# Kernel optimization log

Measured on AMD Instinct MI355X. Metric: run time of the kernel, lower is better.

Reference implementation:

```python
import jax, jax.numpy as jnp
import numpy as np

B, S, DIM = 2, 2048, 2048
H, DN, DR, DV, L = 16, 128, 64, 128, 512  # heads, nope, rope, v, kv_lora_rank
EPS = 1e-5


def setup_inputs() -> dict:
    key = jax.random.key(0)
    ks = jax.random.split(key, 12)
    x = jax.random.normal(ks[0], (B, S, DIM), dtype=jnp.float32)
    # rotary tables (DeepSeek-style: theta = 10000^{-2i/d})
    inv_freq = 1.0 / (10000.0 ** (jnp.arange(0, DR, 2, dtype=jnp.float32) / DR))
    ang = jnp.arange(S, dtype=jnp.float32)[:, None] * inv_freq[None, :]  # [S, DR/2]
    freqs_cos = jnp.cos(ang)
    freqs_sin = jnp.sin(ang)
    w = 0.02
    wq_w = jax.random.normal(ks[1], (H * (DN + DR), DIM), dtype=jnp.float32) * w
    wq_b = jnp.zeros((H * (DN + DR),), dtype=jnp.float32)
    wkv_a_w = jax.random.normal(ks[2], (L + DR, DIM), dtype=jnp.float32) * w
    wkv_a_b = jnp.zeros((L + DR,), dtype=jnp.float32)
    kv_norm_g = jnp.ones((L,), dtype=jnp.float32)
    kv_norm_b = jnp.zeros((L,), dtype=jnp.float32)
    wkv_b_w = jax.random.normal(ks[3], (H * (DN + DV), L), dtype=jnp.float32) * w
    wo_w = jax.random.normal(ks[4], (DIM, H * DV), dtype=jnp.float32) * w
    wo_b = jnp.zeros((DIM,), dtype=jnp.float32)
    return {"x": x, "start_pos": 0, "freqs_cos": freqs_cos, "freqs_sin": freqs_sin,
            "wq_w": wq_w, "wq_b": wq_b, "wkv_a_w": wkv_a_w, "wkv_a_b": wkv_a_b,
            "kv_norm_g": kv_norm_g, "kv_norm_b": kv_norm_b, "wkv_b_w": wkv_b_w,
            "wo_w": wo_w, "wo_b": wo_b}


def _rope(t, cos, sin):
    # t: [B, S, n, DR] interpreted as interleaved (re, im) pairs
    tr = t.reshape(*t.shape[:-1], DR // 2, 2)
    re, im = tr[..., 0], tr[..., 1]
    c = cos[None, :, None, :]
    s = sin[None, :, None, :]
    out = jnp.stack([re * c - im * s, re * s + im * c], axis=-1)
    return out.reshape(t.shape)


def _layernorm(v, g, b):
    mu = jnp.mean(v, axis=-1, keepdims=True)
    var = jnp.mean(jnp.square(v - mu), axis=-1, keepdims=True)
    return (v - mu) * jax.lax.rsqrt(var + EPS) * g + b


def reference(x, start_pos, freqs_cos, freqs_sin, wq_w, wq_b, wkv_a_w, wkv_a_b,
              kv_norm_g, kv_norm_b, wkv_b_w, wo_w, wo_b):
    bsz, seqlen, _ = x.shape
    scale = (DN + DR) ** -0.5
    # q projection
    q = (x @ wq_w.T + wq_b).reshape(bsz, seqlen, H, DN + DR)
    q_nope, q_pe = q[..., :DN], q[..., DN:]
    q_pe = _rope(q_pe, freqs_cos, freqs_sin)
    # kv projection
    kv_full = x @ wkv_a_w.T + wkv_a_b
    kv, k_pe = kv_full[..., :L], kv_full[..., L:]
    k_pe = _rope(k_pe[:, :, None, :], freqs_cos, freqs_sin)[:, :, 0, :]  # [B,S,DR]
    kvn = _layernorm(kv, kv_norm_g, kv_norm_b)  # compressed kv cache entries [B,S,L]
    wkv_b = wkv_b_w.reshape(H, DN + DV, L)
    # absorption: fold wkv_b's k-part into q_nope
    q_abs = jnp.einsum('bshd,hdc->bshc', q_nope, wkv_b[:, :DN])
    scores = (jnp.einsum('bshc,btc->bsht', q_abs, kvn)
              + jnp.einsum('bshr,btr->bsht', q_pe, k_pe)) * scale
    # causal mask (query global pos = start_pos + s, key pos = t)
    qpos = jnp.arange(seqlen) + start_pos
    tpos = jnp.arange(seqlen)
    causal = qpos[:, None] >= tpos[None, :]  # [S, T]
    scores = jnp.where(causal[None, :, None, :], scores, -jnp.inf)
    p = jax.nn.softmax(scores.astype(jnp.float32), axis=-1).astype(x.dtype)
    # compressed attention output then un-absorb v
    ctx = jnp.einsum('bsht,btc->bshc', p, kvn)
    out = jnp.einsum('bshc,hdc->bshd', ctx, wkv_b[:, -DV:])
    return out.reshape(bsz, seqlen, H * DV) @ wo_w.T + wo_b
```

## Files before the change

kernel.cpp:

```cpp
#include <hip/hip_runtime.h>
#include <stdint.h>

typedef __attribute__((ext_vector_type(8))) __bf16 bf16x8;
typedef __attribute__((ext_vector_type(4))) float  f32x4;
typedef __attribute__((ext_vector_type(8))) unsigned short u16x8;
typedef __attribute__((ext_vector_type(2))) unsigned int u32x2;
typedef __attribute__((ext_vector_type(4))) unsigned int u32x4;

typedef __attribute__((address_space(1))) void AS1void;
typedef __attribute__((address_space(3))) void AS3void;
typedef __attribute__((address_space(3))) const unsigned char AS3c;

__device__ __forceinline__ float b2f(unsigned short u) {
  unsigned x = ((unsigned)u) << 16; float f; __builtin_memcpy(&f, &x, 4); return f;
}
__device__ __forceinline__ unsigned short f2b(float f) {
  unsigned x; __builtin_memcpy(&x, &f, 4);
  unsigned r = (x + 0x7fffu + ((x >> 16) & 1u)) >> 16;
  return (unsigned short)r;
}
__device__ __forceinline__ void gload16(const void* g, void* l) {
  __builtin_amdgcn_global_load_lds((AS1void*)(void*)g, (AS3void*)l, 16, 0, 0);
}
__device__ __forceinline__ bf16x8 mk8(u32x2 a, u32x2 b) {
  u32x4 t; t[0] = a[0]; t[1] = a[1]; t[2] = b[0]; t[3] = b[1];
  bf16x8 r; __builtin_memcpy(&r, &t, 16); return r;
}
template<int OFF>
__device__ __forceinline__ u32x2 tr_read(AS3c* vp) {
  u32x2 r;
  asm volatile("ds_read_b64_tr_b16 %0, %1 offset:%2"
               : "=&v"(r) : "v"(vp), "n"(OFF));
  return r;
}

__global__ __launch_bounds__(256) void k_cast(const float* __restrict__ in,
                                              unsigned short* __restrict__ out, long n) {
  long i = ((long)blockIdx.x * 256 + threadIdx.x) * 4;
  if (i >= n) return;
  float4 v = *(const float4*)(in + i);
  ushort4 o;
  o.x = f2b(v.x); o.y = f2b(v.y); o.z = f2b(v.z); o.w = f2b(v.w);
  *(ushort4*)(out + i) = o;
}

__global__ __launch_bounds__(256) void k_prep_wkvb(const float* __restrict__ wkvb,
                                                   unsigned short* __restrict__ kT,
                                                   unsigned short* __restrict__ vv) {
  long i = (long)blockIdx.x * 256 + threadIdx.x;
  {
    int d = (int)(i & 127); long r = i >> 7; int c = (int)(r & 511); int h = (int)(r >> 9);
    kT[i] = f2b(wkvb[((long)(h * 256 + d)) * 512 + c]);
  }
  {
    int c = (int)(i & 511); long r = i >> 9; int d = (int)(r & 127); int h = (int)(r >> 7);
    vv[i] = f2b(wkvb[((long)(h * 256 + 128 + d)) * 512 + c]);
  }
}

template<int OUTF32, int BIAS>
__global__ __launch_bounds__(256, 4) void k_gemm_bt(
    const unsigned short* __restrict__ A, long lda, long aSb, long aSh,
    const unsigned short* __restrict__ B, long ldb, long bSb, long bSh,
    void* __restrict__ Cp, long ldc, long cSb, long cSh,
    const float* __restrict__ bias,
    int M, int N, int K, int zH) {
  __shared__ __align__(16) unsigned short sA[128 * 32];
  __shared__ __align__(16) unsigned short sB[128 * 32];
  const int z = blockIdx.z, zb = z / zH, zh = z % zH;
  const unsigned short* Ab = A + zb * aSb + zh * aSh;
  const unsigned short* Bb = B + zb * bSb + zh * bSh;
  const long cOff = (long)zb * cSb + (long)zh * cSh;
  const int n0 = blockIdx.x * 128, m0 = blockIdx.y * 128;
  const int t = threadIdx.x, w = t >> 6, l = t & 63;
  const int wr = (w >> 1) * 64, wc = (w & 1) * 64;
  const int lr = l & 15, lg = l >> 4;
  f32x4 acc[4][4] = {};
  for (int k0 = 0; k0 < K; k0 += 32) {
    #pragma unroll
    for (int cc = 0; cc < 2; ++cc) {
      int c = t + cc * 256;
      int row = c >> 2, col = (c & 3) * 8;
      int ar = m0 + row; ar = ar < M ? ar : M - 1;
      int br = n0 + row; br = br < N ? br : N - 1;
      gload16(Ab + (long)ar * lda + k0 + col, (char*)sA + c * 16);
      gload16(Bb + (long)br * ldb + k0 + col, (char*)sB + c * 16);
    }
    __syncthreads();
    bf16x8 af[4], bf[4];
    #pragma unroll
    for (int i = 0; i < 4; ++i) af[i] = *(const bf16x8*)&sA[(wr + i * 16 + lr) * 32 + lg * 8];
    #pragma unroll
    for (int j = 0; j < 4; ++j) bf[j] = *(const bf16x8*)&sB[(wc + j * 16 + lr) * 32 + lg * 8];
    #pragma unroll
    for (int i = 0; i < 4; ++i)
      #pragma unroll
      for (int j = 0; j < 4; ++j)
        acc[i][j] = __builtin_amdgcn_mfma_f32_16x16x32_bf16(af[i], bf[j], acc[i][j], 0, 0, 0);
    __syncthreads();
  }
  #pragma unroll
  for (int i = 0; i < 4; ++i) {
    #pragma unroll
    for (int r = 0; r < 4; ++r) {
      int row = m0 + wr + i * 16 + lg * 4 + r;
      if (row >= M) continue;
      #pragma unroll
      for (int j = 0; j < 4; ++j) {
        int col = n0 + wc + j * 16 + lr;
        if (col >= N) continue;
        float v = acc[i][j][r];
        if (BIAS) v += bias[col];
        if (OUTF32) ((float*)Cp)[cOff + (long)row * ldc + col] = v;
        else ((unsigned short*)Cp)[cOff + (long)row * ldc + col] = f2b(v);
      }
    }
  }
}

__global__ __launch_bounds__(256) void k_ln(const unsigned short* __restrict__ kvb,
                                            const float* __restrict__ g,
                                            const float* __restrict__ be,
                                            unsigned short* __restrict__ kcat) {
  const int w = threadIdx.x >> 6, l = threadIdx.x & 63;
  const long row = (long)blockIdx.x * 4 + w;
  const unsigned short* src = kvb + row * 576 + l * 8;
  u16x8 v = *(const u16x8*)src;
  float f[8]; float s = 0.f, s2 = 0.f;
  #pragma unroll
  for (int j = 0; j < 8; ++j) { f[j] = b2f(v[j]); s += f[j]; s2 += f[j] * f[j]; }
  #pragma unroll
  for (int m = 1; m < 64; m <<= 1) { s += __shfl_xor(s, m); s2 += __shfl_xor(s2, m); }
  float mu = s * (1.f / 512.f);
  float var = s2 * (1.f / 512.f) - mu * mu;
  float rs = rsqrtf(var + 1e-5f);
  u16x8 o;
  #pragma unroll
  for (int j = 0; j < 8; ++j) {
    int c = l * 8 + j;
    o[j] = f2b((f[j] - mu) * rs * g[c] + be[c]);
  }
  *(u16x8*)(kcat + row * 576 + l * 8) = o;
}

__global__ __launch_bounds__(256) void k_rope_k(const unsigned short* __restrict__ kvb,
                                                const float* __restrict__ fc,
                                                const float* __restrict__ fs,
                                                unsigned short* __restrict__ kcat) {
  int i = blockIdx.x * 256 + threadIdx.x;
  int p = i & 31; int r = i >> 5;
  int s = r & 2047; int b = r >> 11;
  long base = ((long)(b * 2048 + s)) * 576 + 512 + 2 * p;
  float re = b2f(kvb[base]), im = b2f(kvb[base + 1]);
  float c = fc[s * 32 + p], sn = fs[s * 32 + p];
  kcat[base] = f2b(re * c - im * sn);
  kcat[base + 1] = f2b(re * sn + im * c);
}

__global__ __launch_bounds__(256) void k_rope_q(const unsigned short* __restrict__ qfull,
                                                const float* __restrict__ fc,
                                                const float* __restrict__ fs,
                                                unsigned short* __restrict__ qcat) {
  long i = (long)blockIdx.x * 256 + threadIdx.x;
  int p = (int)(i & 31); long r = i >> 5;
  int h = (int)(r & 15); r >>= 4;
  int s = (int)(r & 2047); int b = (int)(r >> 11);
  const unsigned short* src = qfull + ((long)(b * 2048 + s)) * 3072 + h * 192 + 128 + 2 * p;
  float re = b2f(src[0]), im = b2f(src[1]);
  float c = fc[s * 32 + p], sn = fs[s * 32 + p];
  unsigned short* dst = qcat + ((long)((b * 16 + h) * 2048 + s)) * 576 + 512 + 2 * p;
  dst[0] = f2b(re * c - im * sn);
  dst[1] = f2b(re * sn + im * c);
}

__global__ __launch_bounds__(256, 2) void k_attn(
    const unsigned short* __restrict__ qcat,
    const unsigned short* __restrict__ kcat,
    unsigned short* __restrict__ ctx,
    const int* __restrict__ spp) {
  __shared__ __align__(16) char smem[41248];
  const int id = blockIdx.x;
  const int rr = id & 7;
  const int b = rr >> 2;
  const int local = (id >> 3) * 4 + (rr & 3);
  const int qb = 31 - (local >> 4);
  const int h = local & 15;
  const int t = threadIdx.x, w = t >> 6, l = t & 63;
  const int lq = l & 15, hh = l >> 4;
  const int sp = spp[0];
  const long bh = (long)(b * 16 + h);
  const long qrow0 = bh * 2048 + qb * 64 + w * 16;
  const float scale = 0.07216878364870323f;

  bf16x8 qf[18];
  #pragma unroll
  for (int kk = 0; kk < 18; ++kk)
    qf[kk] = *(const bf16x8*)&qcat[(qrow0 + lq) * 576 + kk * 32 + hh * 8];

  f32x4 acc[8][4];
  #pragma unroll
  for (int i = 0; i < 8; ++i)
    #pragma unroll
    for (int j = 0; j < 4; ++j) acc[i][j] = (f32x4){0.f, 0.f, 0.f, 0.f};
  float mrun = -1e30f, lrun = 0.f;
  const int qg = qb * 64 + w * 16 + lq + sp;
  int tmax = qb * 64 + 63 + sp; if (tmax > 2047) tmax = 2047;

  const unsigned short* kbase = kcat + (long)b * 2048 * 576;

  unsigned short* sP = (unsigned short*)(smem + 36864);
  float* sAl = (float*)(smem + 40960);
  int* sNeed = (int*)(smem + 41216);
  const int qrow = w * 16 + lq;
  const int xq = ((qrow >> 1) & 3) << 4;
  const int vcol = (hh * 16) ^ (((lq >> 1) & 3) << 4);
  const int kq = ((lq >> 2) << 7) + ((lq & 3) << 5) + ((hh & 1) << 4) + ((hh >> 1) << 10);

  for (int t0 = 0; t0 <= tmax; t0 += 32) {
    #pragma unroll
    for (int cc = 0; cc < 9; ++cc) {
      int c = t + cc * 256;
      int tt = ((c >> 3) & 7) * 4 + ((c >> 1) & 3);
      int gc = (c >> 6) * 16 + (c & 1) * 8;
      gload16(kbase + (long)(t0 + tt) * 576 + gc, smem + c * 16);
    }
    asm volatile("s_waitcnt vmcnt(0)" ::: "memory");
    __builtin_amdgcn_sched_barrier(0);
    __builtin_amdgcn_s_barrier();
    __builtin_amdgcn_sched_barrier(0);

    f32x4 sc[2];
    sc[0] = (f32x4){0.f,0.f,0.f,0.f}; sc[1] = (f32x4){0.f,0.f,0.f,0.f};
    __builtin_amdgcn_s_setprio(1);
    #pragma unroll
    for (int tf = 0; tf < 2; ++tf) {
      const char* rb = smem + kq + tf * 512;
      #pragma unroll
      for (int kk = 0; kk < 18; ++kk) {
        bf16x8 kf = *(const bf16x8*)(rb + kk * 2048);
        sc[tf] = __builtin_amdgcn_mfma_f32_16x16x32_bf16(kf, qf[kk], sc[tf], 0, 0, 0);
      }
    }
    __builtin_amdgcn_s_setprio(0);

    float v[2][4];
    float mt = -1e30f;
    #pragma unroll
    for (int tf = 0; tf < 2; ++tf)
      #pragma unroll
      for (int r = 0; r < 4; ++r) {
        int tg = t0 + tf * 16 + 4 * hh + r;
        v[tf][r] = (tg <= qg) ? sc[tf][r] * scale : -1e30f;
        mt = fmaxf(mt, v[tf][r]);
      }
    mt = fmaxf(mt, __shfl_xor(mt, 16));
    mt = fmaxf(mt, __shfl_xor(mt, 32));
    float al = 1.f;
    unsigned long long needb = __ballot(mt > mrun + 8.f);
    if (needb) {
      float mn = fmaxf(mrun, mt);
      al = __expf(mrun - mn);
      mrun = mn;
      lrun *= al;
    }
    float sr = 0.f;
    #pragma unroll
    for (int tf = 0; tf < 2; ++tf) {
      ushort4 pk;
      float e0 = __expf(v[tf][0] - mrun);
      float e1 = __expf(v[tf][1] - mrun);
      float e2 = __expf(v[tf][2] - mrun);
      float e3 = __expf(v[tf][3] - mrun);
      sr += (e0 + e1) + (e2 + e3);
      pk.x = f2b(e0); pk.y = f2b(e1); pk.z = f2b(e2); pk.w = f2b(e3);
      *(ushort4*)((char*)sP + qrow * 64 + ((32 * tf + 8 * hh) ^ xq)) = pk;
    }
    sr += __shfl_xor(sr, 16);
    sr += __shfl_xor(sr, 32);
    lrun += sr;
    if (l < 16) sAl[w * 16 + l] = al;
    if (l == 0) sNeed[w] = needb ? 1 : 0;
    asm volatile("s_waitcnt lgkmcnt(0)" ::: "memory");
    __builtin_amdgcn_sched_barrier(0);
    __builtin_amdgcn_s_barrier();
    __builtin_amdgcn_sched_barrier(0);

    int needAny = sNeed[0] | sNeed[1] | sNeed[2] | sNeed[3];
    if (needAny) {
      float a4[4];
      #pragma unroll
      for (int q2 = 0; q2 < 4; ++q2) a4[q2] = sAl[q2 * 16 + lq];
      #pragma unroll
      for (int cb = 0; cb < 8; ++cb)
        #pragma unroll
        for (int q2 = 0; q2 < 4; ++q2) acc[cb][q2] *= a4[q2];
    }
    bf16x8 pf0 = *(const bf16x8*)((char*)sP + (0 * 16 + lq) * 64 + vcol);
    bf16x8 pf1 = *(const bf16x8*)((char*)sP + (1 * 16 + lq) * 64 + vcol);
    bf16x8 pf2 = *(const bf16x8*)((char*)sP + (2 * 16 + lq) * 64 + vcol);
    bf16x8 pf3 = *(const bf16x8*)((char*)sP + (3 * 16 + lq) * 64 + vcol);
    __builtin_amdgcn_sched_barrier(0);
    AS3c* vp3 = (AS3c*)(smem + (w * 8192) + hh * 256 + lq * 8);
    u32x2 A0, A1, B0, B1, C0, C1, D0, D1;
    #define TRR2(d0, d1, CB) do { \
      d0 = tr_read<(CB) * 1024>(vp3); \
      d1 = tr_read<(CB) * 1024 + 128>(vp3); } while (0)
    #define PVC(CB, E0, E1) do { \
      bf16x8 vf = mk8(E0, E1); \
      acc[CB][0] = __builtin_amdgcn_mfma_f32_16x16x32_bf16(vf, pf0, acc[CB][0], 0, 0, 0); \
      acc[CB][1] = __builtin_amdgcn_mfma_f32_16x16x32_bf16(vf, pf1, acc[CB][1], 0, 0, 0); \
      acc[CB][2] = __builtin_amdgcn_mfma_f32_16x16x32_bf16(vf, pf2, acc[CB][2], 0, 0, 0); \
      acc[CB][3] = __builtin_amdgcn_mfma_f32_16x16x32_bf16(vf, pf3, acc[CB][3], 0, 0, 0); } while (0)
    TRR2(A0, A1, 0); TRR2(B0, B1, 1);
    TRR2(C0, C1, 2); TRR2(D0, D1, 3);
    asm volatile("s_waitcnt lgkmcnt(4)" ::: "memory");
    __builtin_amdgcn_sched_barrier(0);
    __builtin_amdgcn_s_setprio(1);
    PVC(0, A0, A1); PVC(1, B0, B1);
    __builtin_amdgcn_s_setprio(0);
    TRR2(A0, A1, 4); TRR2(B0, B1, 5);
    asm volatile("s_waitcnt lgkmcnt(4)" ::: "memory");
    __builtin_amdgcn_sched_barrier(0);
    __builtin_amdgcn_s_setprio(1);
    PVC(2, C0, C1); PVC(3, D0, D1);
    __builtin_amdgcn_s_setprio(0);
    TRR2(C0, C1, 6); TRR2(D0, D1, 7);
    asm volatile("s_waitcnt lgkmcnt(4)" ::: "memory");
    __builtin_amdgcn_sched_barrier(0);
    __builtin_amdgcn_s_setprio(1);
    PVC(4, A0, A1); PVC(5, B0, B1);
    __builtin_amdgcn_s_setprio(0);
    asm volatile("s_waitcnt lgkmcnt(0)" ::: "memory");
    __builtin_amdgcn_sched_barrier(0);
    __builtin_amdgcn_s_setprio(1);
    PVC(6, C0, C1); PVC(7, D0, D1);
    __builtin_amdgcn_s_setprio(0);
    #undef TRR2
    #undef PVC
    __builtin_amdgcn_sched_barrier(0);
    __builtin_amdgcn_s_barrier();
    __builtin_amdgcn_sched_barrier(0);
  }

  if (l < 16) sAl[w * 16 + l] = lrun;
  __syncthreads();
  float linv[4];
  #pragma unroll
  for (int q2 = 0; q2 < 4; ++q2) linv[q2] = 1.0f / sAl[q2 * 16 + lq];
  unsigned short* eb = (unsigned short*)smem;
  unsigned short* Co = ctx + (bh * 2048 + qb * 64) * 512;
  #pragma unroll
  for (int p = 0; p < 2; ++p) {
    __syncthreads();
    #pragma unroll
    for (int cb = 0; cb < 8; ++cb) {
      const int c0 = w * 128 + cb * 16 + hh * 4;
      #pragma unroll
      for (int q2 = 0; q2 < 2; ++q2) {
        int qq = p * 2 + q2;
        f32x4 a = acc[cb][qq];
        ushort4 o;
        o.x = f2b(a[0] * linv[qq]); o.y = f2b(a[1] * linv[qq]);
        o.z = f2b(a[2] * linv[qq]); o.w = f2b(a[3] * linv[qq]);
        *(ushort4*)&eb[(q2 * 16 + lq) * 528 + c0] = o;
      }
    }
    __syncthreads();
    #pragma unroll
    for (int i = 0; i < 8; ++i) {
      int id2 = t + i * 256;
      int row = id2 >> 6, col = (id2 & 63) * 8;
      *(u16x8*)&Co[(long)(p * 32 + row) * 512 + col] = *(const u16x8*)&eb[row * 528 + col];
    }
  }
}

extern "C" void kernel_launch(void* const* d_in, const int* in_sizes, int n_in,
                              void* d_out, int out_size, void* d_ws, size_t ws_size,
                              hipStream_t stream) {
  const float* x      = (const float*)d_in[0];
  const int*   sp     = (const int*)d_in[1];
  const float* fcos   = (const float*)d_in[2];
  const float* fsin   = (const float*)d_in[3];
  const float* wq_w   = (const float*)d_in[4];
  const float* wq_b   = (const float*)d_in[5];
  const float* wkva_w = (const float*)d_in[6];
  const float* wkva_b = (const float*)d_in[7];
  const float* lng    = (const float*)d_in[8];
  const float* lnb    = (const float*)d_in[9];
  const float* wkvb_w = (const float*)d_in[10];
  const float* wo_w   = (const float*)d_in[11];
  const float* wo_b   = (const float*)d_in[12];
  float* out = (float*)d_out;

  if (ws_size < 171180032) return;

  char* ws = (char*)d_ws;
  unsigned short* xb     = (unsigned short*)(ws + 0);
  unsigned short* wqbf   = (unsigned short*)(ws + 16777216);
  unsigned short* qfull  = (unsigned short*)(ws + 29360128);
  unsigned short* ctx    = (unsigned short*)(ws + 0);
  unsigned short* wkvabf = (unsigned short*)(ws + 67108864);
  unsigned short* wkvbkT = (unsigned short*)(ws + 69468160);
  unsigned short* wkvbv  = (unsigned short*)(ws + 71565312);
  unsigned short* wobf   = (unsigned short*)(ws + 73662464);
  unsigned short* kvbf   = (unsigned short*)(ws + 82051072);
  unsigned short* kcat   = (unsigned short*)(ws + 86769664);
  unsigned short* qcat   = (unsigned short*)(ws + 95682560);
  unsigned short* outh   = qcat;

  k_cast<<<8192, 256, 0, stream>>>(x, xb, 8388608L);
  k_cast<<<6144, 256, 0, stream>>>(wq_w, wqbf, 6291456L);
  k_cast<<<1152, 256, 0, stream>>>(wkva_w, wkvabf, 1179648L);
  k_cast<<<4096, 256, 0, stream>>>(wo_w, wobf, 4194304L);
  k_prep_wkvb<<<4096, 256, 0, stream>>>(wkvb_w, wkvbkT, wkvbv);

  k_gemm_bt<0, 1><<<dim3(24, 32, 1), 256, 0, stream>>>(
      xb, 2048, 0, 0, wqbf, 2048, 0, 0, qfull, 3072, 0, 0, wq_b, 4096, 3072, 2048, 1);
  k_gemm_bt<0, 1><<<dim3(5, 32, 1), 256, 0, stream>>>(
      xb, 2048, 0, 0, wkvabf, 2048, 0, 0, kvbf, 576, 0, 0, wkva_b, 4096, 576, 2048, 1);

  k_ln<<<1024, 256, 0, stream>>>(kvbf, lng, lnb, kcat);
  k_rope_k<<<512, 256, 0, stream>>>(kvbf, fcos, fsin, kcat);
  k_rope_q<<<16384, 256, 0, stream>>>(qfull, fcos, fsin, qcat);

  k_gemm_bt<0, 0><<<dim3(4, 16, 32), 256, 0, stream>>>(
      qfull, 3072, (long)2048 * 3072, 192,
      wkvbkT, 128, 0, (long)512 * 128,
      qcat, 576, (long)16 * 2048 * 576, (long)2048 * 576,
      nullptr, 2048, 512, 128, 16);

  k_attn<<<dim3(1024, 1, 1), 256, 0, stream>>>(qcat, kcat, ctx, sp);

  k_gemm_bt<0, 0><<<dim3(1, 16, 32), 256, 0, stream>>>(
      ctx, 512, (long)16 * 2048 * 512, (long)2048 * 512,
      wkvbv, 512, 0, (long)128 * 512,
      outh, 2048, (long)2048 * 2048, 128,
      nullptr, 2048, 128, 512, 16);

  k_gemm_bt<1, 1><<<dim3(16, 32, 1), 256, 0, stream>>>(
      outh, 2048, 0, 0, wobf, 2048, 0, 0, out, 2048, 0, 0, wo_b, 4096, 2048, 2048, 1);
}
```

Baseline: 635.3 us.

## Double attention key tile to 64 tokens per iteration in MLA kernel

Each attention loop iteration now stages 64 key/value rows (instead of 32) into LDS, halving the number of loop iterations, global-load waits and block barriers per KV pass. The QK loop is reordered to iterate over the contraction dimension outermost, the P tile widens to 128 bytes per row with a new XOR swizzle, and PV runs as two 32-token halves. An extra barrier is inserted after QK, and the epilogue writes all 64 output rows in one pass. LDS grows to about 74 KB, which may reduce blocks per CU versus the 2-wave launch bound, and causal blocks now process more masked tokens on the diagonal.

```diff
diff --git a/kernel.cpp b/kernel.cpp
--- a/kernel.cpp
+++ b/kernel.cpp
@@ -178,7 +178,7 @@
     const unsigned short* __restrict__ kcat,
     unsigned short* __restrict__ ctx,
     const int* __restrict__ spp) {
-  __shared__ __align__(16) char smem[41248];
+  __shared__ __align__(16) char smem[74112];
   const int id = blockIdx.x;
   const int rr = id & 7;
   const int b = rr >> 2;
@@ -208,45 +208,49 @@
 
   const unsigned short* kbase = kcat + (long)b * 2048 * 576;
 
-  unsigned short* sP = (unsigned short*)(smem + 36864);
-  float* sAl = (float*)(smem + 40960);
-  int* sNeed = (int*)(smem + 41216);
+  unsigned short* sP = (unsigned short*)(smem + 65536);
+  float* sAl = (float*)(smem + 73728);
+  int* sNeed = (int*)(smem + 73984);
   const int qrow = w * 16 + lq;
-  const int xq = ((qrow >> 1) & 3) << 4;
-  const int vcol = (hh * 16) ^ (((lq >> 1) & 3) << 4);
-  const int kq = ((lq >> 2) << 7) + ((lq & 3) << 5) + ((hh & 1) << 4) + ((hh >> 1) << 10);
-
-  for (int t0 = 0; t0 <= tmax; t0 += 32) {
-    #pragma unroll
-    for (int cc = 0; cc < 9; ++cc) {
-      int c = t + cc * 256;
-      int tt = ((c >> 3) & 7) * 4 + ((c >> 1) & 3);
-      int gc = (c >> 6) * 16 + (c & 1) * 8;
-      gload16(kbase + (long)(t0 + tt) * 576 + gc, smem + c * 16);
+  const int xq = (qrow & 7) << 4;
+  const int kq = ((hh >> 1) << 11) + ((lq >> 2) << 7) + ((lq & 3) << 5) + ((hh & 1) << 4);
+
+  for (int t0 = 0; t0 <= tmax; t0 += 64) {
+    #pragma unroll
+    for (int cc = 0; cc < 18; ++cc) {
+      int c2 = t + cc * 256;
+      int tt = ((c2 >> 3) & 15) * 4 + ((c2 >> 1) & 3);
+      int gc = (c2 >> 7) * 16 + (c2 & 1) * 8;
+      gload16(kbase + (long)(t0 + tt) * 576 + gc, smem + c2 * 16);
     }
     asm volatile("s_waitcnt vmcnt(0)" ::: "memory");
     __builtin_amdgcn_sched_barrier(0);
     __builtin_amdgcn_s_barrier();
     __builtin_amdgcn_sched_barrier(0);
 
-    f32x4 sc[2];
-    sc[0] = (f32x4){0.f,0.f,0.f,0.f}; sc[1] = (f32x4){0.f,0.f,0.f,0.f};
+    f32x4 sc[4];
+    #pragma unroll
+    for (int tf = 0; tf < 4; ++tf) sc[tf] = (f32x4){0.f, 0.f, 0.f, 0.f};
     __builtin_amdgcn_s_setprio(1);
     #pragma unroll
-    for (int tf = 0; tf < 2; ++tf) {
-      const char* rb = smem + kq + tf * 512;
-      #pragma unroll
-      for (int kk = 0; kk < 18; ++kk) {
-        bf16x8 kf = *(const bf16x8*)(rb + kk * 2048);
+    for (int kk = 0; kk < 18; ++kk) {
+      const char* rb = smem + kq + kk * 4096;
+      #pragma unroll
+      for (int tf = 0; tf < 4; ++tf) {
+        bf16x8 kf = *(const bf16x8*)(rb + tf * 512);
         sc[tf] = __builtin_amdgcn_mfma_f32_16x16x32_bf16(kf, qf[kk], sc[tf], 0, 0, 0);
       }
     }
     __builtin_amdgcn_s_setprio(0);
-
-    float v[2][4];
+    asm volatile("s_waitcnt lgkmcnt(0)" ::: "memory");
+    __builtin_amdgcn_sched_barrier(0);
+    __builtin_amdgcn_s_barrier();
+    __builtin_amdgcn_sched_barrier(0);
+
+    float v[4][4];
     float mt = -1e30f;
     #pragma unroll
-    for (int tf = 0; tf < 2; ++tf)
+    for (int tf = 0; tf < 4; ++tf)
       #pragma unroll
       for (int r = 0; r < 4; ++r) {
         int tg = t0 + tf * 16 + 4 * hh + r;
@@ -265,7 +269,7 @@
     }
     float sr = 0.f;
     #pragma unroll
-    for (int tf = 0; tf < 2; ++tf) {
+    for (int tf = 0; tf < 4; ++tf) {
       ushort4 pk;
       float e0 = __expf(v[tf][0] - mrun);
       float e1 = __expf(v[tf][1] - mrun);
@@ -273,7 +277,7 @@
       float e3 = __expf(v[tf][3] - mrun);
       sr += (e0 + e1) + (e2 + e3);
       pk.x = f2b(e0); pk.y = f2b(e1); pk.z = f2b(e2); pk.w = f2b(e3);
-      *(ushort4*)((char*)sP + qrow * 64 + ((32 * tf + 8 * hh) ^ xq)) = pk;
+      *(ushort4*)((char*)sP + qrow * 128 + ((32 * tf + 8 * hh) ^ xq)) = pk;
     }
     sr += __shfl_xor(sr, 16);
     sr += __shfl_xor(sr, 32);
@@ -295,48 +299,51 @@
         #pragma unroll
         for (int q2 = 0; q2 < 4; ++q2) acc[cb][q2] *= a4[q2];
     }
-    bf16x8 pf0 = *(const bf16x8*)((char*)sP + (0 * 16 + lq) * 64 + vcol);
-    bf16x8 pf1 = *(const bf16x8*)((char*)sP + (1 * 16 + lq) * 64 + vcol);
-    bf16x8 pf2 = *(const bf16x8*)((char*)sP + (2 * 16 + lq) * 64 + vcol);
-    bf16x8 pf3 = *(const bf16x8*)((char*)sP + (3 * 16 + lq) * 64 + vcol);
-    __builtin_amdgcn_sched_barrier(0);
-    AS3c* vp3 = (AS3c*)(smem + (w * 8192) + hh * 256 + lq * 8);
-    u32x2 A0, A1, B0, B1, C0, C1, D0, D1;
-    #define TRR2(d0, d1, CB) do { \
-      d0 = tr_read<(CB) * 1024>(vp3); \
-      d1 = tr_read<(CB) * 1024 + 128>(vp3); } while (0)
-    #define PVC(CB, E0, E1) do { \
-      bf16x8 vf = mk8(E0, E1); \
-      acc[CB][0] = __builtin_amdgcn_mfma_f32_16x16x32_bf16(vf, pf0, acc[CB][0], 0, 0, 0); \
-      acc[CB][1] = __builtin_amdgcn_mfma_f32_16x16x32_bf16(vf, pf1, acc[CB][1], 0, 0, 0); \
-      acc[CB][2] = __builtin_amdgcn_mfma_f32_16x16x32_bf16(vf, pf2, acc[CB][2], 0, 0, 0); \
-      acc[CB][3] = __builtin_amdgcn_mfma_f32_16x16x32_bf16(vf, pf3, acc[CB][3], 0, 0, 0); } while (0)
-    TRR2(A0, A1, 0); TRR2(B0, B1, 1);
-    TRR2(C0, C1, 2); TRR2(D0, D1, 3);
-    asm volatile("s_waitcnt lgkmcnt(4)" ::: "memory");
-    __builtin_amdgcn_sched_barrier(0);
-    __builtin_amdgcn_s_setprio(1);
-    PVC(0, A0, A1); PVC(1, B0, B1);
-    __builtin_amdgcn_s_setprio(0);
-    TRR2(A0, A1, 4); TRR2(B0, B1, 5);
-    asm volatile("s_waitcnt lgkmcnt(4)" ::: "memory");
-    __builtin_amdgcn_sched_barrier(0);
-    __builtin_amdgcn_s_setprio(1);
-    PVC(2, C0, C1); PVC(3, D0, D1);
-    __builtin_amdgcn_s_setprio(0);
-    TRR2(C0, C1, 6); TRR2(D0, D1, 7);
-    asm volatile("s_waitcnt lgkmcnt(4)" ::: "memory");
-    __builtin_amdgcn_sched_barrier(0);
-    __builtin_amdgcn_s_setprio(1);
-    PVC(4, A0, A1); PVC(5, B0, B1);
-    __builtin_amdgcn_s_setprio(0);
-    asm volatile("s_waitcnt lgkmcnt(0)" ::: "memory");
-    __builtin_amdgcn_sched_barrier(0);
-    __builtin_amdgcn_s_setprio(1);
-    PVC(6, C0, C1); PVC(7, D0, D1);
-    __builtin_amdgcn_s_setprio(0);
-    #undef TRR2
-    #undef PVC
+    AS3c* vp3 = (AS3c*)(smem + w * 16384 + hh * 256 + lq * 8);
+    #pragma unroll
+    for (int ts = 0; ts < 2; ++ts) {
+      bf16x8 pf0 = *(const bf16x8*)((char*)sP + (0 * 16 + lq) * 128 + ((64 * ts + 16 * hh) ^ ((lq & 7) << 4)));
+      bf16x8 pf1 = *(const bf16x8*)((char*)sP + (1 * 16 + lq) * 128 + ((64 * ts + 16 * hh) ^ ((lq & 7) << 4)));
+      bf16x8 pf2 = *(const bf16x8*)((char*)sP + (2 * 16 + lq) * 128 + ((64 * ts + 16 * hh) ^ ((lq & 7) << 4)));
+      bf16x8 pf3 = *(const bf16x8*)((char*)sP + (3 * 16 + lq) * 128 + ((64 * ts + 16 * hh) ^ ((lq & 7) << 4)));
+      __builtin_amdgcn_sched_barrier(0);
+      u32x2 A0, A1, B0, B1, C0, C1, D0, D1;
+      #define TRR2(d0, d1, CB) do { \
+        d0 = tr_read<(CB) * 2048>(vp3 + ts * 1024); \
+        d1 = tr_read<(CB) * 2048 + 128>(vp3 + ts * 1024); } while (0)
+      #define PVC(CB, E0, E1) do { \
+        bf16x8 vf = mk8(E0, E1); \
+        acc[CB][0] = __builtin_amdgcn_mfma_f32_16x16x32_bf16(vf, pf0, acc[CB][0], 0, 0, 0); \
+        acc[CB][1] = __builtin_amdgcn_mfma_f32_16x16x32_bf16(vf, pf1, acc[CB][1], 0, 0, 0); \
+        acc[CB][2] = __builtin_amdgcn_mfma_f32_16x16x32_bf16(vf, pf2, acc[CB][2], 0, 0, 0); \
+        acc[CB][3] = __builtin_amdgcn_mfma_f32_16x16x32_bf16(vf, pf3, acc[CB][3], 0, 0, 0); } while (0)
+      TRR2(A0, A1, 0); TRR2(B0, B1, 1);
+      TRR2(C0, C1, 2); TRR2(D0, D1, 3);
+      asm volatile("s_waitcnt lgkmcnt(4)" ::: "memory");
+      __builtin_amdgcn_sched_barrier(0);
+      __builtin_amdgcn_s_setprio(1);
+      PVC(0, A0, A1); PVC(1, B0, B1);
+      __builtin_amdgcn_s_setprio(0);
+      TRR2(A0, A1, 4); TRR2(B0, B1, 5);
+      asm volatile("s_waitcnt lgkmcnt(4)" ::: "memory");
+      __builtin_amdgcn_sched_barrier(0);
+      __builtin_amdgcn_s_setprio(1);
+      PVC(2, C0, C1); PVC(3, D0, D1);
+      __builtin_amdgcn_s_setprio(0);
+      TRR2(C0, C1, 6); TRR2(D0, D1, 7);
+      asm volatile("s_waitcnt lgkmcnt(4)" ::: "memory");
+      __builtin_amdgcn_sched_barrier(0);
+      __builtin_amdgcn_s_setprio(1);
+      PVC(4, A0, A1); PVC(5, B0, B1);
+      __builtin_amdgcn_s_setprio(0);
+      asm volatile("s_waitcnt lgkmcnt(0)" ::: "memory");
+      __builtin_amdgcn_sched_barrier(0);
+      __builtin_amdgcn_s_setprio(1);
+      PVC(6, C0, C1); PVC(7, D0, D1);
+      __builtin_amdgcn_s_setprio(0);
+      #undef TRR2
+      #undef PVC
+    }
     __builtin_amdgcn_sched_barrier(0);
     __builtin_amdgcn_s_barrier();
     __builtin_amdgcn_sched_barrier(0);
@@ -348,30 +355,25 @@
   #pragma unroll
   for (int q2 = 0; q2 < 4; ++q2) linv[q2] = 1.0f / sAl[q2 * 16 + lq];
   unsigned short* eb = (unsigned short*)smem;
+  #pragma unroll
+  for (int cb = 0; cb < 8; ++cb) {
+    const int c0 = w * 128 + cb * 16 + hh * 4;
+    #pragma unroll
+    for (int q2 = 0; q2 < 4; ++q2) {
+      f32x4 a = acc[cb][q2];
+      ushort4 o;
+      o.x = f2b(a[0] * linv[q2]); o.y = f2b(a[1] * linv[q2]);
+      o.z = f2b(a[2] * linv[q2]); o.w = f2b(a[3] * linv[q2]);
+      *(ushort4*)&eb[(q2 * 16 + lq) * 528 + c0] = o;
+    }
+  }
+  __syncthreads();
   unsigned short* Co = ctx + (bh * 2048 + qb * 64) * 512;
   #pragma unroll
-  for (int p = 0; p < 2; ++p) {
-    __syncthreads();
-    #pragma unroll
-    for (int cb = 0; cb < 8; ++cb) {
-      const int c0 = w * 128 + cb * 16 + hh * 4;
-      #pragma unroll
-      for (int q2 = 0; q2 < 2; ++q2) {
-        int qq = p * 2 + q2;
-        f32x4 a = acc[cb][qq];
-        ushort4 o;
-        o.x = f2b(a[0] * linv[qq]); o.y = f2b(a[1] * linv[qq]);
-        o.z = f2b(a[2] * linv[qq]); o.w = f2b(a[3] * linv[qq]);
-        *(ushort4*)&eb[(q2 * 16 + lq) * 528 + c0] = o;
-      }
-    }
-    __syncthreads();
-    #pragma unroll
-    for (int i = 0; i < 8; ++i) {
-      int id2 = t + i * 256;
-      int row = id2 >> 6, col = (id2 & 63) * 8;
-      *(u16x8*)&Co[(long)(p * 32 + row) * 512 + col] = *(const u16x8*)&eb[row * 528 + col];
-    }
+  for (int i = 0; i < 16; ++i) {
+    int id2 = t + i * 256;
+    int row = id2 >> 6, col = (id2 & 63) * 8;
+    *(u16x8*)&Co[(long)row * 512 + col] = *(const u16x8*)&eb[row * 528 + col];
   }
 }
 
```

Result: no change. 626.5 us (-1.4%).
